# Kernel optimization log

Hardware: AMD Instinct MI355X
Metric: run time of the kernel (lower is better)

## Reference

```python
import jax, jax.numpy as jnp
import numpy as np

SCALE_XY = 0.1
SCALE_WH = 0.2
CRITERIA = 0.5        # NMS IoU threshold
MAX_OUTPUT = 100      # max detections per image
SCORE_THRESH = 0.05   # pre-NMS score threshold
MIN_SIZE = 1.0 / 300.0  # min box width/height
TOP_K = 400           # fixed-size candidate set for jit-compatible NMS


def setup_inputs() -> dict:
    key = jax.random.key(0)
    k1, k2, k3, k4 = jax.random.split(key, 4)
    N, C, B = 32, 81, 8732
    bboxes_in = jax.random.normal(k1, (N, 4, B), jnp.float32)
    scores_in = jax.random.normal(k2, (N, C, B), jnp.float32)
    # synthetic but realistic default boxes: centers in [0,1], wh in [0.02,0.4]
    xy = jax.random.uniform(k3, (B, 2), jnp.float32)
    wh = jax.random.uniform(k4, (B, 2), jnp.float32, minval=0.02, maxval=0.4)
    dboxes_xywh = jnp.concatenate([xy, wh], axis=-1)[None]  # [1, B, 4]
    return {"bboxes_in": bboxes_in, "scores_in": scores_in, "dboxes_xywh": dboxes_xywh}


def _scale_back(bboxes_in, scores_in, dboxes):
    # bboxes_in [N,4,B] -> [N,B,4]; scores_in [N,C,B] -> [N,B,C]
    bb = jnp.transpose(bboxes_in, (0, 2, 1))
    sc = jnp.transpose(scores_in, (0, 2, 1))
    xy = SCALE_XY * bb[..., :2] * dboxes[..., 2:] + dboxes[..., :2]
    wh = jnp.exp(SCALE_WH * bb[..., 2:]) * dboxes[..., 2:]
    ltrb = jnp.concatenate([xy - 0.5 * wh, xy + 0.5 * wh], axis=-1)  # [N,B,4]
    probs = jax.nn.softmax(sc, axis=-1)                               # [N,B,C]
    return ltrb, probs


def _decode_single(boxes, probs):
    # boxes [B,4] (ltrb), probs [B,C]
    B, C = probs.shape
    boxes = jnp.clip(boxes, 0.0, 1.0)
    sc = probs[:, 1:]  # drop background class 0 -> [B, C-1]
    w = boxes[:, 2] - boxes[:, 0]
    h = boxes[:, 3] - boxes[:, 1]
    valid_box = (w >= MIN_SIZE) & (h >= MIN_SIZE)
    valid = (sc > SCORE_THRESH) & valid_box[:, None]
    flat = jnp.where(valid, sc, -1.0).reshape(-1)  # [B*(C-1)], row-major: box then class
    vals, idx = jax.lax.top_k(flat, TOP_K)         # sorted desc by score
    box_idx = idx // (C - 1)
    labels = idx % (C - 1) + 1                     # class ids 1..C-1
    cboxes = boxes[box_idx]                        # [K,4]
    cscores = sc.reshape(-1)[idx]                  # [K] (differentiable gather)
    kvalid = vals > 0.0
    # batched_nms trick: offset boxes by label so different classes never overlap
    off = labels.astype(boxes.dtype)[:, None] * 2.0  # coords are in [0,1]
    ob = cboxes + off
    lt = jnp.maximum(ob[:, None, :2], ob[None, :, :2])
    rb = jnp.minimum(ob[:, None, 2:], ob[None, :, 2:])
    inter = jnp.prod(jnp.clip(rb - lt, 0.0, None), axis=-1)         # [K,K]
    area = jnp.prod(jnp.clip(ob[:, 2:] - ob[:, :2], 0.0, None), axis=-1)
    iou = inter / jnp.maximum(area[:, None] + area[None, :] - inter, 1e-12)
    order = jnp.arange(TOP_K)

    def body(i, keep):
        sup = keep[i] & (iou[i] > CRITERIA) & (order > i)
        return keep & ~sup

    keep = jax.lax.fori_loop(0, TOP_K, body, kvalid)
    final = jnp.where(keep, cscores, -1.0)
    out_s, out_i = jax.lax.top_k(final, MAX_OUTPUT)  # first MAX_OUTPUT kept, score order
    ok = out_s > 0.0
    out_boxes = jnp.where(ok[:, None], cboxes[out_i], 0.0)
    out_labels = jnp.where(ok, labels[out_i], 0)
    out_scores = jnp.where(ok, cscores[out_i], 0.0)
    return out_boxes, out_labels, out_scores


def reference(bboxes_in, scores_in, dboxes_xywh):
    ltrb, probs = _scale_back(bboxes_in, scores_in, dboxes_xywh)
    boxes, labels, scores = jax.vmap(_decode_single)(ltrb, probs)
    return boxes, labels, scores  # [N,100,4], [N,100] int, [N,100]
```

## Files before the change

kernel.cpp:

```cpp
#include <hip/hip_runtime.h>
#include <cstdint>
#include <cstddef>

#define NIMG 32
#define NCLS 81
#define NC1  80
#define NBOX 8732
#define CAP  65536
#define TOPK 400
#define MAXOUT 100
#define KW   7
#define COLCAP 2048
#define BDEC 256
#define BSEL 512
#define CNTSTRIDE 16
#define RSTRIDE 409

__device__ __forceinline__ unsigned int f2sort(float f) {
    unsigned int u = __float_as_uint(f);
    return (u & 0x80000000u) ? ~u : (u | 0x80000000u);
}

__global__ __launch_bounds__(BDEC) void k_decode(const float* __restrict__ bboxes,
        const float* __restrict__ scores, const float* __restrict__ dbox,
        float4* __restrict__ oboxes, uint2* __restrict__ cand, int* __restrict__ cnt) {
    int n = blockIdx.y;
    int b = blockIdx.x * BDEC + threadIdx.x;
    int lane = threadIdx.x & 63;
    bool live = (b < NBOX);
    int bs = live ? b : 0;

    const float* sp = scores + (size_t)n * NCLS * NBOX + bs;
    float sc[NCLS];
    #pragma unroll
    for (int c = 0; c < NCLS; ++c) sc[c] = sp[(size_t)c * NBOX];

    bool go = false;
    float l = 0.f, tt = 0.f, r = 0.f, bo = 0.f;
    if (live) {
        const float* bp = bboxes + (size_t)n * 4 * NBOX + b;
        float bx = bp[0], by = bp[NBOX], bw = bp[2 * NBOX], bh = bp[3 * NBOX];
        float4 d = reinterpret_cast<const float4*>(dbox)[b];
        float cx = 0.1f * bx * d.z + d.x;
        float cy = 0.1f * by * d.w + d.y;
        float ww = expf(0.2f * bw) * d.z;
        float hh = expf(0.2f * bh) * d.w;
        l = cx - 0.5f * ww;  tt = cy - 0.5f * hh;
        r = cx + 0.5f * ww;  bo = cy + 0.5f * hh;
        l = fminf(fmaxf(l, 0.f), 1.f);  tt = fminf(fmaxf(tt, 0.f), 1.f);
        r = fminf(fmaxf(r, 0.f), 1.f);  bo = fminf(fmaxf(bo, 0.f), 1.f);
        const float MINS = 1.0f / 300.0f;
        go = (r - l >= MINS) && (bo - tt >= MINS);
    }

    float m = -3.4e38f;
    #pragma unroll
    for (int c = 0; c < NCLS; ++c) m = fmaxf(m, sc[c]);

    float ss = 0.f;
    #pragma unroll
    for (int c = 0; c < NCLS; ++c) { sc[c] = expf(sc[c] - m); ss += sc[c]; }

    float t05 = 0.05f * ss;
    float thi = t05 * 1.000001f;
    float tlo = t05 * 0.999999f;
    unsigned long long mlo = 0ull;
    unsigned int       mhi = 0u;
    #pragma unroll
    for (int c = 1; c < NCLS; ++c) {
        float e = sc[c];
        bool bit;
        if (e > thi)       bit = true;
        else if (e < tlo)  bit = false;
        else               bit = (e / ss > 0.05f);
        if (go && bit) {
            if (c <= 64) mlo |= 1ull << (c - 1);
            else         mhi |= 1u << (c - 65);
        }
    }

    int nc = (int)__popcll(mlo) + __popc(mhi);
    int incl = nc;
    #pragma unroll
    for (int off = 1; off < 64; off <<= 1) {
        int u = __shfl_up(incl, off);
        if (lane >= off) incl += u;
    }
    int excl = incl - nc;
    int tot = __shfl(incl, 63);
    int base = 0;
    if (lane == 0 && tot > 0) base = atomicAdd(&cnt[n * CNTSTRIDE], tot);
    base = __shfl(base, 0);

    if (nc > 0) {
        int pos = base + excl;
        uint2* cp = cand + (size_t)n * CAP;
        #pragma unroll
        for (int c = 1; c < NCLS; ++c) {
            bool bit = (c <= 64) ? (((mlo >> (c - 1)) & 1ull) != 0)
                                 : (((mhi >> (c - 65)) & 1u) != 0);
            if (bit) {
                float p = sc[c] / ss;
                if (pos < CAP) cp[pos] = make_uint2(__float_as_uint(p),
                                                    (unsigned)(b * NC1 + (c - 1)));
                ++pos;
            }
        }
    }

    if (live && nc > 0) oboxes[(size_t)n * NBOX + b] = make_float4(l, tt, r, bo);
}

__device__ void bitonic_desc(unsigned long long* arr, int nn, int tid, int nt) {
    for (int k = 2; k <= nn; k <<= 1) {
        for (int j = k >> 1; j > 0; j >>= 1) {
            __syncthreads();
            for (int i = tid; i < nn; i += nt) {
                int ixj = i ^ j;
                if (ixj > i) {
                    unsigned long long a = arr[i], b = arr[ixj];
                    bool desc = ((i & k) == 0);
                    bool sw = desc ? (a < b) : (a > b);
                    if (sw) { arr[i] = b; arr[ixj] = a; }
                }
            }
        }
    }
    __syncthreads();
}

__global__ __launch_bounds__(BSEL) void k_topk(const float4* __restrict__ boxes,
        const uint2* __restrict__ cand, const int* __restrict__ cnt,
        float* __restrict__ g_sc, float4* __restrict__ g_cb, int* __restrict__ g_lab,
        float4* __restrict__ g_ob, float* __restrict__ g_ar, int* __restrict__ g_nsel) {
    __shared__ int hist[1024];
    __shared__ unsigned long long keys[COLCAP];
    __shared__ int s_T, s_pos;

    int n = blockIdx.x;
    int tid = threadIdx.x;
    int lane = tid & 63;
    unsigned long long lmlt = (1ull << lane) - 1ull;
    int M = cnt[n * CNTSTRIDE]; if (M > CAP) M = CAP;
    const uint2* cp = cand + (size_t)n * CAP;

    hist[tid] = 0; hist[tid + BSEL] = 0;
    if (tid == 0) s_pos = 0;
    __syncthreads();

    for (int i = tid; i < M; i += BSEL) {
        unsigned int bits = cp[i].x;
        int bk = (int)(bits >> 16) - 0x3D00;
        bk = max(0, min(1023, bk));
        atomicAdd(&hist[bk], 1);
    }
    __syncthreads();

    if (tid < 64) {
        int sl = 0;
        #pragma unroll
        for (int t = 0; t < 16; ++t) sl += hist[tid * 16 + t];
        int incl = sl;
        #pragma unroll
        for (int off = 1; off < 64; off <<= 1) {
            int v = __shfl_down(incl, off);
            if (tid + off < 64) incl += v;
        }
        int xl = incl - sl;
        int tc = -1, cum = xl;
        for (int t = 15; t >= 0; --t) {
            cum += hist[tid * 16 + t];
            if (cum >= TOPK) { tc = tid * 16 + t; break; }
        }
        #pragma unroll
        for (int off = 32; off > 0; off >>= 1)
            tc = max(tc, __shfl_xor(tc, off));
        if (tid == 0) s_T = max(tc, 0);
    }
    __syncthreads();
    int T = s_T;

    int iters = (M + BSEL - 1) / BSEL;
    for (int it = 0; it < iters; ++it) {
        int i = it * BSEL + tid;
        bool pred = false; unsigned long long key = 0ull;
        if (i < M) {
            uint2 e = cp[i];
            int bk = (int)(e.x >> 16) - 0x3D00;
            bk = max(0, min(1023, bk));
            if (bk >= T) {
                pred = true;
                key = ((unsigned long long)e.x << 32) | (unsigned int)(~e.y);
            }
        }
        unsigned long long mask = __ballot(pred);
        int base = 0;
        if (lane == 0) {
            int cw = (int)__popcll(mask);
            if (cw) base = atomicAdd(&s_pos, cw);
        }
        base = __shfl(base, 0);
        if (pred) {
            int pos = base + (int)__popcll(mask & lmlt);
            if (pos < COLCAP) keys[pos] = key;
        }
    }
    __syncthreads();
    int ncol = min(s_pos, COLCAP);

    int nsort = 512;
    while (nsort < ncol) nsort <<= 1;
    for (int i = ncol + tid; i < nsort; i += BSEL) keys[i] = 0ull;
    __syncthreads();
    bitonic_desc(keys, nsort, tid, BSEL);

    int nsel = min(TOPK, ncol);
    if (tid < TOPK) {
        int i = tid;
        float sc = -1.0f; float4 cb = make_float4(0.f, 0.f, 0.f, 0.f);
        int lab = 0; float4 ob = cb; float ar = 0.f;
        if (i < nsel) {
            unsigned long long key = keys[i];
            unsigned int bits = (unsigned int)(key >> 32);
            unsigned int flat = ~(unsigned int)key;
            int bb = (int)(flat / NC1);
            lab = (int)(flat - (unsigned)bb * NC1) + 1;
            sc = __uint_as_float(bits);
            cb = boxes[(size_t)n * NBOX + bb];
            float off = 2.0f * (float)lab;
            ob = make_float4(cb.x + off, cb.y + off, cb.z + off, cb.w + off);
            ar = fmaxf(ob.z - ob.x, 0.f) * fmaxf(ob.w - ob.y, 0.f);
        }
        size_t gi = (size_t)n * TOPK + i;
        g_sc[gi] = sc; g_cb[gi] = cb; g_lab[gi] = lab; g_ob[gi] = ob; g_ar[gi] = ar;
    }
    if (tid == 0) g_nsel[n] = nsel;
}

__global__ __launch_bounds__(256) void k_iou(const float4* __restrict__ g_ob,
        const float* __restrict__ g_ar, const int* __restrict__ g_nsel,
        unsigned long long* __restrict__ g_rows) {
    __shared__ float4 s_ob[TOPK];
    __shared__ float  s_ar[TOPK];
    int n = blockIdx.y, w = blockIdx.x;
    int tid = threadIdx.x;
    for (int i = tid; i < TOPK; i += 256) {
        s_ob[i] = g_ob[(size_t)n * TOPK + i];
        s_ar[i] = g_ar[(size_t)n * TOPK + i];
    }
    __syncthreads();
    int nsel = g_nsel[n];
    int j0 = w * 64;
    unsigned long long* gr = g_rows + ((size_t)n * KW + w) * TOPK;
    for (int i = tid; i < TOPK; i += 256) {
        unsigned long long cur = 0ull;
        if (i < nsel) {
            float4 oi = s_ob[i]; float ai = s_ar[i];
            int jend = min(j0 + 64, nsel);
            for (int j = j0; j < jend; ++j) {
                if (j > i) {
                    float4 oj = s_ob[j];
                    float lx = fmaxf(oi.x, oj.x), ly = fmaxf(oi.y, oj.y);
                    float rx = fminf(oi.z, oj.z), ry = fminf(oi.w, oj.w);
                    float inter = fmaxf(rx - lx, 0.f) * fmaxf(ry - ly, 0.f);
                    float uni = fmaxf(ai + s_ar[j] - inter, 1e-12f);
                    cur |= ((unsigned long long)(inter / uni > 0.5f)) << (j - j0);
                }
            }
        }
        gr[i] = cur;
    }
}

__global__ __launch_bounds__(512) void k_nms(const unsigned long long* __restrict__ g_rows,
        const float* __restrict__ g_sc, const float4* __restrict__ g_cb,
        const int* __restrict__ g_lab, const int* __restrict__ g_nsel,
        float* __restrict__ out) {
    __shared__ unsigned long long rows[KW * RSTRIDE];
    __shared__ unsigned long long nz[8];
    __shared__ unsigned long long s_keep[KW];
    __shared__ int pc[KW + 1];

    int n = blockIdx.x;
    int tid = threadIdx.x;
    int lane = tid & 63;
    int nsel = g_nsel[n];

    const unsigned long long* gr = g_rows + (size_t)n * KW * TOPK;
    for (int t = tid; t < KW * TOPK; t += 512) {
        int w = t / TOPK, i = t - w * TOPK;
        rows[w * RSTRIDE + i] = gr[t];
    }
    __syncthreads();

    {
        unsigned long long v = 0ull;
        if (tid < TOPK) {
            #pragma unroll
            for (int w = 0; w < KW; ++w) v |= rows[w * RSTRIDE + tid];
        }
        unsigned long long bal = __ballot(v != 0ull);
        if (lane == 0) nz[tid >> 6] = bal;
    }
    __syncthreads();

    if (tid < 64) {
        unsigned long long keepw = 0ull;
        if (lane < KW) {
            int lo = lane << 6;
            keepw = (nsel >= lo + 64) ? ~0ull
                  : (nsel <= lo ? 0ull : ((1ull << (nsel - lo)) - 1ull));
        }
        #pragma unroll
        for (int w = 0; w < KW; ++w) {
            unsigned long long nzw = nz[w];
            while (nzw) {
                int bq = (int)__ffsll((long long)nzw) - 1;
                nzw &= nzw - 1;
                int i = (w << 6) + bq;
                unsigned long long row = (lane < KW) ? rows[lane * RSTRIDE + i] : 0ull;
                unsigned long long kwv = __shfl(keepw, w);
                if ((kwv >> bq) & 1ull) keepw &= ~row;
            }
        }
        if (lane < KW) s_keep[lane] = keepw;
    }
    __syncthreads();

    if (tid == 0) {
        int acc = 0;
        #pragma unroll
        for (int w = 0; w < KW; ++w) { pc[w] = acc; acc += (int)__popcll(s_keep[w]); }
        pc[KW] = acc;
    }
    __syncthreads();

    float* obox = out;
    float* olab = out + (size_t)NIMG * MAXOUT * 4;
    float* osco = out + (size_t)NIMG * MAXOUT * 5;
    int nkept = pc[KW];

    if (tid < TOPK) {
        unsigned long long kw = s_keep[tid >> 6];
        bool kb = (kw >> (tid & 63)) & 1ull;
        if (kb) {
            int rank = pc[tid >> 6] + (int)__popcll(kw & ((1ull << (tid & 63)) - 1ull));
            if (rank < MAXOUT) {
                size_t gi = (size_t)n * TOPK + tid;
                float4 cb = g_cb[gi];
                size_t bo_ = ((size_t)n * MAXOUT + rank) * 4;
                obox[bo_ + 0] = cb.x; obox[bo_ + 1] = cb.y;
                obox[bo_ + 2] = cb.z; obox[bo_ + 3] = cb.w;
                olab[(size_t)n * MAXOUT + rank] = (float)g_lab[gi];
                osco[(size_t)n * MAXOUT + rank] = g_sc[gi];
            }
        }
    }
    if (tid < MAXOUT && tid >= nkept) {
        size_t bo_ = ((size_t)n * MAXOUT + tid) * 4;
        obox[bo_ + 0] = 0.f; obox[bo_ + 1] = 0.f; obox[bo_ + 2] = 0.f; obox[bo_ + 3] = 0.f;
        olab[(size_t)n * MAXOUT + tid] = 0.f;
        osco[(size_t)n * MAXOUT + tid] = 0.f;
    }
}

extern "C" void kernel_launch(void* const* d_in, const int* in_sizes, int n_in,
                              void* d_out, int out_size, void* d_ws, size_t ws_size,
                              hipStream_t stream) {
    (void)in_sizes; (void)n_in; (void)out_size; (void)ws_size;
    const float* bboxes = (const float*)d_in[0];
    const float* scores = (const float*)d_in[1];
    const float* dbox   = (const float*)d_in[2];
    float* out = (float*)d_out;

    char* ws = (char*)d_ws;
    size_t off = 0;
    float4* oboxes = (float4*)(ws + off); off += (size_t)NIMG * NBOX * sizeof(float4);
    int* cnt = (int*)(ws + off); off += (size_t)NIMG * CNTSTRIDE * sizeof(int);
    uint2* cand = (uint2*)(ws + off); off += (size_t)NIMG * CAP * sizeof(uint2);
    float* g_sc = (float*)(ws + off); off += (size_t)NIMG * TOPK * sizeof(float);
    float4* g_cb = (float4*)(ws + off); off += (size_t)NIMG * TOPK * sizeof(float4);
    int* g_lab = (int*)(ws + off); off += (size_t)NIMG * TOPK * sizeof(int);
    float4* g_ob = (float4*)(ws + off); off += (size_t)NIMG * TOPK * sizeof(float4);
    float* g_ar = (float*)(ws + off); off += (size_t)NIMG * TOPK * sizeof(float);
    int* g_nsel = (int*)(ws + off); off += 256;
    unsigned long long* g_rows = (unsigned long long*)(ws + off);
    off += (size_t)NIMG * KW * TOPK * sizeof(unsigned long long);

    hipMemsetAsync(cnt, 0, NIMG * CNTSTRIDE * sizeof(int), stream);

    int gx = (NBOX + BDEC - 1) / BDEC;
    k_decode<<<dim3(gx, NIMG), BDEC, 0, stream>>>(bboxes, scores, dbox, oboxes, cand, cnt);
    k_topk<<<NIMG, BSEL, 0, stream>>>(oboxes, cand, cnt, g_sc, g_cb, g_lab, g_ob, g_ar, g_nsel);
    k_iou<<<dim3(KW, NIMG), 256, 0, stream>>>(g_ob, g_ar, g_nsel, g_rows);
    k_nms<<<NIMG, 512, 0, stream>>>(g_rows, g_sc, g_cb, g_lab, g_nsel, out);
}
```

Measured before the change: 116.8 us.

## Fuse top-k, IoU bitmask and NMS kernels into one per-image kernel

Merges the top-k selection, IoU suppression-mask computation and greedy NMS into a single kernel per image, keeping candidate boxes, scores, labels and mask rows in shared memory instead of round-tripping through global workspace. This removes two kernel launches and the global writes and reads between stages. The IoU matrix is now computed by only 32 blocks of 512 threads instead of 224 blocks, which lowers parallelism for that stage and raises shared-memory use per block. It also adds a launch-bounds occupancy hint to the decode kernel.

```diff
diff --git a/kernel.cpp b/kernel.cpp
--- a/kernel.cpp
+++ b/kernel.cpp
@@ -21,7 +21,7 @@
     return (u & 0x80000000u) ? ~u : (u | 0x80000000u);
 }
 
-__global__ __launch_bounds__(BDEC) void k_decode(const float* __restrict__ bboxes,
+__global__ __launch_bounds__(BDEC, 2) void k_decode(const float* __restrict__ bboxes,
         const float* __restrict__ scores, const float* __restrict__ dbox,
         float4* __restrict__ oboxes, uint2* __restrict__ cand, int* __restrict__ cnt) {
     int n = blockIdx.y;
@@ -106,9 +106,8 @@
                 ++pos;
             }
         }
-    }
-
-    if (live && nc > 0) oboxes[(size_t)n * NBOX + b] = make_float4(l, tt, r, bo);
+        oboxes[(size_t)n * NBOX + b] = make_float4(l, tt, r, bo);
+    }
 }
 
 __device__ void bitonic_desc(unsigned long long* arr, int nn, int tid, int nt) {
@@ -129,12 +128,20 @@
     __syncthreads();
 }
 
-__global__ __launch_bounds__(BSEL) void k_topk(const float4* __restrict__ boxes,
+__global__ __launch_bounds__(BSEL) void k_select(const float4* __restrict__ boxes,
         const uint2* __restrict__ cand, const int* __restrict__ cnt,
-        float* __restrict__ g_sc, float4* __restrict__ g_cb, int* __restrict__ g_lab,
-        float4* __restrict__ g_ob, float* __restrict__ g_ar, int* __restrict__ g_nsel) {
+        float* __restrict__ out) {
     __shared__ int hist[1024];
     __shared__ unsigned long long keys[COLCAP];
+    __shared__ float  s_score[TOPK];
+    __shared__ float4 s_cbox[TOPK];
+    __shared__ int    s_label[TOPK];
+    __shared__ float4 s_ob[TOPK];
+    __shared__ float  s_ar[TOPK];
+    __shared__ unsigned long long rows[KW * RSTRIDE];
+    __shared__ unsigned long long nz[8];
+    __shared__ unsigned long long s_keep[KW];
+    __shared__ int pc[KW + 1];
     __shared__ int s_T, s_pos;
 
     int n = blockIdx.x;
@@ -217,45 +224,36 @@
     int nsel = min(TOPK, ncol);
     if (tid < TOPK) {
         int i = tid;
-        float sc = -1.0f; float4 cb = make_float4(0.f, 0.f, 0.f, 0.f);
-        int lab = 0; float4 ob = cb; float ar = 0.f;
         if (i < nsel) {
             unsigned long long key = keys[i];
             unsigned int bits = (unsigned int)(key >> 32);
             unsigned int flat = ~(unsigned int)key;
             int bb = (int)(flat / NC1);
-            lab = (int)(flat - (unsigned)bb * NC1) + 1;
-            sc = __uint_as_float(bits);
-            cb = boxes[(size_t)n * NBOX + bb];
+            int lab = (int)(flat - (unsigned)bb * NC1) + 1;
+            float sc = __uint_as_float(bits);
+            float4 cb = boxes[(size_t)n * NBOX + bb];
+            s_score[i] = sc; s_cbox[i] = cb; s_label[i] = lab;
             float off = 2.0f * (float)lab;
-            ob = make_float4(cb.x + off, cb.y + off, cb.z + off, cb.w + off);
-            ar = fmaxf(ob.z - ob.x, 0.f) * fmaxf(ob.w - ob.y, 0.f);
-        }
-        size_t gi = (size_t)n * TOPK + i;
-        g_sc[gi] = sc; g_cb[gi] = cb; g_lab[gi] = lab; g_ob[gi] = ob; g_ar[gi] = ar;
-    }
-    if (tid == 0) g_nsel[n] = nsel;
-}
-
-__global__ __launch_bounds__(256) void k_iou(const float4* __restrict__ g_ob,
-        const float* __restrict__ g_ar, const int* __restrict__ g_nsel,
-        unsigned long long* __restrict__ g_rows) {
-    __shared__ float4 s_ob[TOPK];
-    __shared__ float  s_ar[TOPK];
-    int n = blockIdx.y, w = blockIdx.x;
-    int tid = threadIdx.x;
-    for (int i = tid; i < TOPK; i += 256) {
-        s_ob[i] = g_ob[(size_t)n * TOPK + i];
-        s_ar[i] = g_ar[(size_t)n * TOPK + i];
-    }
-    __syncthreads();
-    int nsel = g_nsel[n];
-    int j0 = w * 64;
-    unsigned long long* gr = g_rows + ((size_t)n * KW + w) * TOPK;
-    for (int i = tid; i < TOPK; i += 256) {
+            float4 ob = make_float4(cb.x + off, cb.y + off, cb.z + off, cb.w + off);
+            s_ob[i] = ob;
+            s_ar[i] = fmaxf(ob.z - ob.x, 0.f) * fmaxf(ob.w - ob.y, 0.f);
+        } else {
+            s_score[i] = -1.0f;
+            s_cbox[i] = make_float4(0.f, 0.f, 0.f, 0.f);
+            s_label[i] = 0;
+            s_ob[i] = make_float4(0.f, 0.f, 0.f, 0.f);
+            s_ar[i] = 0.f;
+        }
+    }
+    __syncthreads();
+
+    for (int t = tid; t < TOPK * KW; t += BSEL) {
+        int w = t / TOPK;
+        int i = t - w * TOPK;
         unsigned long long cur = 0ull;
         if (i < nsel) {
             float4 oi = s_ob[i]; float ai = s_ar[i];
+            int j0 = w * 64;
             int jend = min(j0 + 64, nsel);
             for (int j = j0; j < jend; ++j) {
                 if (j > i) {
@@ -268,28 +266,7 @@
                 }
             }
         }
-        gr[i] = cur;
-    }
-}
-
-__global__ __launch_bounds__(512) void k_nms(const unsigned long long* __restrict__ g_rows,
-        const float* __restrict__ g_sc, const float4* __restrict__ g_cb,
-        const int* __restrict__ g_lab, const int* __restrict__ g_nsel,
-        float* __restrict__ out) {
-    __shared__ unsigned long long rows[KW * RSTRIDE];
-    __shared__ unsigned long long nz[8];
-    __shared__ unsigned long long s_keep[KW];
-    __shared__ int pc[KW + 1];
-
-    int n = blockIdx.x;
-    int tid = threadIdx.x;
-    int lane = tid & 63;
-    int nsel = g_nsel[n];
-
-    const unsigned long long* gr = g_rows + (size_t)n * KW * TOPK;
-    for (int t = tid; t < KW * TOPK; t += 512) {
-        int w = t / TOPK, i = t - w * TOPK;
-        rows[w * RSTRIDE + i] = gr[t];
+        rows[w * RSTRIDE + i] = cur;
     }
     __syncthreads();
 
@@ -346,13 +323,12 @@
         if (kb) {
             int rank = pc[tid >> 6] + (int)__popcll(kw & ((1ull << (tid & 63)) - 1ull));
             if (rank < MAXOUT) {
-                size_t gi = (size_t)n * TOPK + tid;
-                float4 cb = g_cb[gi];
+                float4 cb = s_cbox[tid];
                 size_t bo_ = ((size_t)n * MAXOUT + rank) * 4;
                 obox[bo_ + 0] = cb.x; obox[bo_ + 1] = cb.y;
                 obox[bo_ + 2] = cb.z; obox[bo_ + 3] = cb.w;
-                olab[(size_t)n * MAXOUT + rank] = (float)g_lab[gi];
-                osco[(size_t)n * MAXOUT + rank] = g_sc[gi];
+                olab[(size_t)n * MAXOUT + rank] = (float)s_label[tid];
+                osco[(size_t)n * MAXOUT + rank] = s_score[tid];
             }
         }
     }
@@ -378,20 +354,10 @@
     float4* oboxes = (float4*)(ws + off); off += (size_t)NIMG * NBOX * sizeof(float4);
     int* cnt = (int*)(ws + off); off += (size_t)NIMG * CNTSTRIDE * sizeof(int);
     uint2* cand = (uint2*)(ws + off); off += (size_t)NIMG * CAP * sizeof(uint2);
-    float* g_sc = (float*)(ws + off); off += (size_t)NIMG * TOPK * sizeof(float);
-    float4* g_cb = (float4*)(ws + off); off += (size_t)NIMG * TOPK * sizeof(float4);
-    int* g_lab = (int*)(ws + off); off += (size_t)NIMG * TOPK * sizeof(int);
-    float4* g_ob = (float4*)(ws + off); off += (size_t)NIMG * TOPK * sizeof(float4);
-    float* g_ar = (float*)(ws + off); off += (size_t)NIMG * TOPK * sizeof(float);
-    int* g_nsel = (int*)(ws + off); off += 256;
-    unsigned long long* g_rows = (unsigned long long*)(ws + off);
-    off += (size_t)NIMG * KW * TOPK * sizeof(unsigned long long);
 
     hipMemsetAsync(cnt, 0, NIMG * CNTSTRIDE * sizeof(int), stream);
 
     int gx = (NBOX + BDEC - 1) / BDEC;
     k_decode<<<dim3(gx, NIMG), BDEC, 0, stream>>>(bboxes, scores, dbox, oboxes, cand, cnt);
-    k_topk<<<NIMG, BSEL, 0, stream>>>(oboxes, cand, cnt, g_sc, g_cb, g_lab, g_ob, g_ar, g_nsel);
-    k_iou<<<dim3(KW, NIMG), 256, 0, stream>>>(g_ob, g_ar, g_nsel, g_rows);
-    k_nms<<<NIMG, 512, 0, stream>>>(g_rows, g_sc, g_cb, g_lab, g_nsel, out);
-}
+    k_select<<<NIMG, BSEL, 0, stream>>>(oboxes, cand, cnt, out);
+}
```

Result: slower. 134.5 us (+15.2%).
